# Kernel tuning notes

Measured on AMD Instinct MI355X. Metric: run time of the kernel, lower is better.

## Reference

```python
import jax, jax.numpy as jnp
import numpy as np

LEVEL_SHAPES = ((100, 100), (50, 50), (25, 25))  # (H, W) per feature level
B, S, D, H, L, P, FFN = 2, 13125, 256, 8, 3, 4, 1024
Dh = D // H


def setup_inputs() -> dict:
    key = jax.random.key(0)
    ks = jax.random.split(key, 24)

    def rn(k, shape, s=0.02):
        return jax.random.normal(k, shape, jnp.float32) * s

    starts = np.cumsum([0] + [h * w for h, w in LEVEL_SHAPES])[:-1]
    return {
        "x": jax.random.normal(ks[0], (B, S, D), jnp.float32),
        "pos_embed": jax.random.normal(ks[1], (B, S, D), jnp.float32) * 0.1,
        "ref_points": jax.random.uniform(ks[2], (B, S, L, 2), jnp.float32),
        "W_off": rn(ks[3], (D, H * L * P * 2)),
        "b_off": rn(ks[4], (H * L * P * 2,), 0.5),
        "W_attn": rn(ks[5], (D, H * L * P)),
        "b_attn": rn(ks[6], (H * L * P,)),
        "W_val": rn(ks[7], (D, D)),
        "b_val": rn(ks[8], (D,)),
        "W_out": rn(ks[9], (D, D)),
        "b_out": rn(ks[10], (D,)),
        "g1": jnp.ones((D,), jnp.float32),
        "be1": jnp.zeros((D,), jnp.float32),
        "W1": rn(ks[11], (D, FFN)),
        "b1": rn(ks[12], (FFN,)),
        "W2": rn(ks[13], (FFN, D)),
        "b2": rn(ks[14], (D,)),
        "g2": jnp.ones((D,), jnp.float32),
        "be2": jnp.zeros((D,), jnp.float32),
        "level_shapes": jnp.array(LEVEL_SHAPES, jnp.int32),
        "level_start_idx": jnp.array(starts, jnp.int32),
    }


def layer_norm(x, g, b, eps=1e-5):
    m = jnp.mean(x, -1, keepdims=True)
    v = jnp.var(x, -1, keepdims=True)
    return (x - m) * jax.lax.rsqrt(v + eps) * g + b


def bilinear_sample(vl, loc, Hl, Wl):
    # vl: [B,H,S_l,Dh]; loc: [B,H,S,P,2] normalized (x,y) in [0,1]
    # grid_sample semantics: align_corners=False, padding_mode='zeros'
    x = loc[..., 0] * Wl - 0.5
    y = loc[..., 1] * Hl - 0.5
    x0 = jnp.floor(x)
    y0 = jnp.floor(y)
    fx = x - x0
    fy = y - y0
    x0i = x0.astype(jnp.int32)
    y0i = y0.astype(jnp.int32)
    out = 0.0
    for dy, dx, w in ((0, 0, (1 - fx) * (1 - fy)), (0, 1, fx * (1 - fy)),
                      (1, 0, (1 - fx) * fy), (1, 1, fx * fy)):
        xi = x0i + dx
        yi = y0i + dy
        valid = (xi >= 0) & (xi < Wl) & (yi >= 0) & (yi < Hl)
        idx = jnp.clip(yi, 0, Hl - 1) * Wl + jnp.clip(xi, 0, Wl - 1)
        b_, h_, s_, p_ = idx.shape
        g = jnp.take_along_axis(vl, idx.reshape(b_, h_, s_ * p_)[..., None], axis=2)
        g = g.reshape(b_, h_, s_, p_, Dh)
        out = out + g * (w * valid)[..., None]
    return out  # [B,H,S,P,Dh]


def ms_deform_attn(q, x, ref_points, W_off, b_off, W_attn, b_attn, W_val, b_val, W_out, b_out):
    value = (x @ W_val + b_val).reshape(B, S, H, Dh).transpose(0, 2, 1, 3)  # [B,H,S,Dh]
    off = (q @ W_off + b_off).reshape(B, S, H, L, P, 2)
    attn = jax.nn.softmax((q @ W_attn + b_attn).reshape(B, S, H, L * P), axis=-1)
    attn = attn.reshape(B, S, H, L, P).transpose(0, 2, 1, 3, 4)  # [B,H,S,L,P]
    # offset normalizer is (W, H) per level
    norm = jnp.array([[w, h] for h, w in LEVEL_SHAPES], jnp.float32)
    loc = ref_points[:, :, None, :, None, :] + off / norm[None, None, None, :, None, :]
    loc = loc.transpose(0, 2, 1, 3, 4, 5)  # [B,H,S,L,P,2]
    s0 = 0
    sampled = []
    for l, (Hl, Wl) in enumerate(LEVEL_SHAPES):
        vl = jax.lax.slice_in_dim(value, s0, s0 + Hl * Wl, axis=2)
        sampled.append(bilinear_sample(vl, loc[:, :, :, l], Hl, Wl))
        s0 += Hl * Wl
    sampled = jnp.stack(sampled, axis=3)  # [B,H,S,L,P,Dh]
    out = jnp.einsum('bhslp,bhslpd->bshd', attn, sampled).reshape(B, S, D)
    return out @ W_out + b_out


def reference(x, pos_embed, ref_points, W_off, b_off, W_attn, b_attn, W_val, b_val,
              W_out, b_out, g1, be1, W1, b1, W2, b2, g2, be2,
              level_shapes, level_start_idx):
    q = x + pos_embed
    attn_out = ms_deform_attn(q, x, ref_points, W_off, b_off, W_attn, b_attn,
                              W_val, b_val, W_out, b_out)
    h1 = layer_norm(x + attn_out, g1, be1)
    ffn = jax.nn.relu(h1 @ W1 + b1) @ W2 + b2
    return layer_norm(h1 + ffn, g2, be2)
```

## Files before the change

### kernel.cpp

```cpp
#include <hip/hip_runtime.h>
#include <hip/hip_bf16.h>

namespace {

constexpr int kB = 2, kS = 13125, kD = 256, kH = 8, kL = 3, kP = 4, kFFN = 1024, kDh = 32;
constexpr int kM = kB * kS;

typedef __attribute__((ext_vector_type(8))) short short8v;
typedef __attribute__((ext_vector_type(4))) float f32x4;

__device__ __forceinline__ float bf2f(unsigned short u) {
  unsigned int x = ((unsigned int)u) << 16;
  return __builtin_bit_cast(float, x);
}
__device__ __forceinline__ unsigned short f2bf(float f) {
  unsigned int u = __builtin_bit_cast(unsigned int, f);
  u += 0x7FFFu + ((u >> 16) & 1u);
  return (unsigned short)(u >> 16);
}

__device__ __forceinline__ void gload_lds16(const void* g, void* l) {
  __builtin_amdgcn_global_load_lds(
      (const __attribute__((address_space(1))) unsigned int*)g,
      (__attribute__((address_space(3))) unsigned int*)l, 16, 0, 0);
}

__global__ __launch_bounds__(256) void wprep_kernel(const float* __restrict__ W,
                                                    unsigned short* __restrict__ Wt,
                                                    int K, int N, int total) {
  int idx = blockIdx.x * 256 + threadIdx.x;
  if (idx >= total) return;
  int n = idx / K, k = idx - n * K;
  float v = (n < N) ? W[(size_t)k * N + n] : 0.f;
  Wt[idx] = f2bf(v);
}

__global__ __launch_bounds__(256) void wprep_comb(const float* __restrict__ Woff,
                                                  const float* __restrict__ Wattn,
                                                  const float* __restrict__ boff,
                                                  const float* __restrict__ battn,
                                                  unsigned short* __restrict__ Wt,
                                                  float* __restrict__ bc) {
  int idx = blockIdx.x * 256 + threadIdx.x;
  if (idx >= 288 * 256) return;
  int n = idx >> 8, k = idx & 255;
  int h = n / 36, j = n - h * 36;
  float v = (j < 24) ? Woff[(size_t)k * 192 + h * 24 + j]
                     : Wattn[(size_t)k * 96 + h * 12 + (j - 24)];
  Wt[idx] = f2bf(v);
  if (idx < 288) {
    int hh = idx / 36, jj = idx - hh * 36;
    bc[idx] = (jj < 24) ? boff[hh * 24 + jj] : battn[hh * 12 + (jj - 24)];
  }
}

__global__ __launch_bounds__(256) void prep_kernel(const float4* __restrict__ x,
                                                   const float4* __restrict__ pos,
                                                   ushort4* __restrict__ xb,
                                                   ushort4* __restrict__ qb, int n4) {
  int i = blockIdx.x * 256 + threadIdx.x;
  if (i < n4) {
    float4 a = x[i], b = pos[i];
    xb[i] = make_ushort4(f2bf(a.x), f2bf(a.y), f2bf(a.z), f2bf(a.w));
    qb[i] = make_ushort4(f2bf(a.x + b.x), f2bf(a.y + b.y),
                         f2bf(a.z + b.z), f2bf(a.w + b.w));
  }
}

template <int EPI, bool OBF, int MI>
__global__ __launch_bounds__(256) void mfma_gemm(const unsigned short* __restrict__ A,
                                                 const unsigned short* __restrict__ Bt,
                                                 const float* __restrict__ bias,
                                                 void* __restrict__ Cp,
                                                 int M, int N, int K) {
  constexpr int BM = MI * 32;
  __shared__ unsigned short smem[2 * 128 * 32];
  unsigned short* As = smem;
  unsigned short* Bs = smem + BM * 32;
  const int tid = threadIdx.x;
  const int w = tid >> 6, lane = tid & 63;
  const int m0 = blockIdx.y * BM, n0 = blockIdx.x * 128;
  const int wr = w >> 1, wc = w & 1;
  const int r_ = lane >> 2, sl = lane & 3;

  f32x4 acc[MI][4] = {};

  for (int k0 = 0; k0 < K; k0 += 32) {
#pragma unroll
    for (int i = 0; i < MI / 2; ++i) {
      const int row = i * 64 + w * 16 + r_;
      const int sg = sl ^ ((row >> 1) & 3);
      int arow = m0 + row;
      arow = arow < M ? arow : M - 1;
      gload_lds16(A + (size_t)arow * K + k0 + sg * 8, &As[(i * 64 + w * 16) * 32]);
    }
#pragma unroll
    for (int i = 0; i < 2; ++i) {
      const int row = i * 64 + w * 16 + r_;
      const int sg = sl ^ ((row >> 1) & 3);
      gload_lds16(Bt + (size_t)(n0 + row) * K + k0 + sg * 8, &Bs[(i * 64 + w * 16) * 32]);
    }
    __syncthreads();
    short8v a[MI], b[4];
#pragma unroll
    for (int mi = 0; mi < MI; ++mi) {
      const int row = wr * (MI * 16) + mi * 16 + (lane & 15);
      const int slot = (lane >> 4) ^ ((row >> 1) & 3);
      a[mi] = *(const short8v*)&As[row * 32 + slot * 8];
    }
#pragma unroll
    for (int ni = 0; ni < 4; ++ni) {
      const int row = wc * 64 + ni * 16 + (lane & 15);
      const int slot = (lane >> 4) ^ ((row >> 1) & 3);
      b[ni] = *(const short8v*)&Bs[row * 32 + slot * 8];
    }
#pragma unroll
    for (int mi = 0; mi < MI; ++mi)
#pragma unroll
      for (int ni = 0; ni < 4; ++ni)
        acc[mi][ni] = __builtin_amdgcn_mfma_f32_16x16x32_bf16(a[mi], b[ni], acc[mi][ni], 0, 0, 0);
    __syncthreads();
  }

  const int cr = lane >> 4, cc = lane & 15;
  if (OBF) {
    unsigned short* Cs = smem;
#pragma unroll
    for (int half = 0; half < MI / 2; ++half) {
      if (MI == 2 || wr == half) {
#pragma unroll
        for (int ni = 0; ni < 4; ++ni) {
          const int col = wc * 64 + ni * 16 + cc;
          const float bv = bias[n0 + col];
#pragma unroll
          for (int mi = 0; mi < MI; ++mi)
#pragma unroll
            for (int r = 0; r < 4; ++r) {
              const int loc = wr * (MI * 16) + mi * 16 + cr * 4 + r - half * 64;
              float v = acc[mi][ni][r] + bv;
              if (EPI == 2) v = fmaxf(v, 0.f);
              const int ch = (col >> 3) ^ (loc & 7);
              Cs[loc * 128 + ch * 8 + (col & 7)] = f2bf(v);
            }
        }
      }
      __syncthreads();
      const int lr = tid >> 4, lc = tid & 15;
#pragma unroll
      for (int pp = 0; pp < 4; ++pp) {
        const int loc = pp * 16 + lr;
        const int grow = m0 + half * 64 + loc;
        const short8v vv = *(const short8v*)&Cs[loc * 128 + ((lc ^ (loc & 7)) * 8)];
        if (grow < M)
          *(short8v*)((unsigned short*)Cp + (size_t)grow * N + n0 + lc * 8) = vv;
      }
      __syncthreads();
    }
  } else {
#pragma unroll
    for (int ni = 0; ni < 4; ++ni) {
      const int col = n0 + wc * 64 + ni * 16 + cc;
      if (col >= N) continue;
      const float bv = bias[col];
#pragma unroll
      for (int mi = 0; mi < MI; ++mi) {
#pragma unroll
        for (int r = 0; r < 4; ++r) {
          const int row = m0 + wr * (MI * 16) + mi * 16 + cr * 4 + r;
          if (row >= M) continue;
          ((float*)Cp)[(size_t)row * N + col] = acc[mi][ni][r] + bv;
        }
      }
    }
  }
}

__global__ __launch_bounds__(256) void sample_kernel(const unsigned short* __restrict__ value,
                                                     const float* __restrict__ oa,
                                                     const float* __restrict__ refp,
                                                     unsigned short* __restrict__ out) {
  const int tid = threadIdx.x;
  const int sub = tid >> 2;
  const int lane = tid & 3;
  const int gi = blockIdx.x * 64 + sub;
  if (gi >= kB * kS * kH) return;
  const int h = gi & 7;
  const int bs = gi >> 3;
  const int b = (bs >= kS) ? 1 : 0;

  const float* op = oa + (size_t)bs * 288 + h * 36;
  const float* al = op + 24;
  float w[12];
  float mx = -1e30f;
#pragma unroll
  for (int i = 0; i < 12; ++i) { w[i] = al[i]; mx = fmaxf(mx, w[i]); }
  float sum = 0.f;
#pragma unroll
  for (int i = 0; i < 12; ++i) { w[i] = expf(w[i] - mx); sum += w[i]; }
  const float inv = 1.f / sum;
#pragma unroll
  for (int i = 0; i < 12; ++i) w[i] *= inv;

  const float* rp = refp + (size_t)bs * (kL * 2);
  const unsigned short* vbase = value + (size_t)b * kS * kD + h * kDh + lane * 8;

  const int LH[3] = {100, 50, 25}, LW[3] = {100, 50, 25}, LS[3] = {0, 10000, 12500};
  float acc[8] = {};
#pragma unroll
  for (int l = 0; l < 3; ++l) {
    const int Wi = LW[l], Hi = LH[l];
    const float Wl = (float)Wi, Hl = (float)Hi;
    const float rxw = rp[l * 2 + 0] * Wl - 0.5f;
    const float ryh = rp[l * 2 + 1] * Hl - 0.5f;
    const unsigned short* lvl = vbase + (size_t)LS[l] * kD;
#pragma unroll
    for (int p = 0; p < 4; ++p) {
      const float ox = op[l * 8 + p * 2 + 0], oy = op[l * 8 + p * 2 + 1];
      const float xf = rxw + ox;
      const float yf = ryh + oy;
      const float x0f = floorf(xf), y0f = floorf(yf);
      const float fx = xf - x0f, fy = yf - y0f;
      const int x0 = (int)x0f, y0 = (int)y0f;
      const int x1 = x0 + 1, y1 = y0 + 1;
      const bool vx0 = (unsigned)x0 < (unsigned)Wi;
      const bool vx1 = (unsigned)x1 < (unsigned)Wi;
      const bool vy0 = (unsigned)y0 < (unsigned)Hi;
      const bool vy1 = (unsigned)y1 < (unsigned)Hi;
      const int cx0 = min(max(x0, 0), Wi - 1), cx1 = min(max(x1, 0), Wi - 1);
      const int cy0 = min(max(y0, 0), Hi - 1), cy1 = min(max(y1, 0), Hi - 1);
      const float aw = w[l * 4 + p];
      const float ax = aw * fx, a0 = aw - ax;
      const float w00 = a0 - a0 * fy, w10 = a0 * fy;
      const float w01 = ax - ax * fy, w11 = ax * fy;
      const float m00 = (vx0 && vy0) ? w00 : 0.f;
      const float m01 = (vx1 && vy0) ? w01 : 0.f;
      const float m10 = (vx0 && vy1) ? w10 : 0.f;
      const float m11 = (vx1 && vy1) ? w11 : 0.f;
      const int ry0 = cy0 * Wi, ry1 = cy1 * Wi;
      const short8v q00 = *(const short8v*)(lvl + ((size_t)(ry0 + cx0) << 8));
      const short8v q01 = *(const short8v*)(lvl + ((size_t)(ry0 + cx1) << 8));
      const short8v q10 = *(const short8v*)(lvl + ((size_t)(ry1 + cx0) << 8));
      const short8v q11 = *(const short8v*)(lvl + ((size_t)(ry1 + cx1) << 8));
#pragma unroll
      for (int c = 0; c < 8; ++c) {
        float s = m00 * bf2f((unsigned short)q00[c]);
        s = fmaf(m01, bf2f((unsigned short)q01[c]), s);
        s = fmaf(m10, bf2f((unsigned short)q10[c]), s);
        s = fmaf(m11, bf2f((unsigned short)q11[c]), s);
        acc[c] += s;
      }
    }
  }
  unsigned short r[8];
#pragma unroll
  for (int c = 0; c < 8; ++c) r[c] = f2bf(acc[c]);
  *(short8v*)(out + (size_t)bs * kD + h * kDh + lane * 8) = *(const short8v*)r;
}

template <int WB>
__global__ __launch_bounds__(256) void lnres_kernel(const float* __restrict__ X,
                                                    const unsigned short* __restrict__ Ab,
                                                    const float* __restrict__ g,
                                                    const float* __restrict__ be,
                                                    float* __restrict__ out,
                                                    unsigned short* __restrict__ outb,
                                                    int rows) {
  const int wid = threadIdx.x >> 6, lane = threadIdx.x & 63;
  const int row = blockIdx.x * 4 + wid;
  if (row >= rows) return;
  const float4 v = ((const float4*)(X + (size_t)row * kD))[lane];
  const ushort4 a4 = ((const ushort4*)(Ab + (size_t)row * kD))[lane];
  float4 t;
  t.x = v.x + bf2f(a4.x);
  t.y = v.y + bf2f(a4.y);
  t.z = v.z + bf2f(a4.z);
  t.w = v.w + bf2f(a4.w);
  float s = t.x + t.y + t.z + t.w;
  float sq = t.x * t.x + t.y * t.y + t.z * t.z + t.w * t.w;
#pragma unroll
  for (int o = 1; o < 64; o <<= 1) {
    s += __shfl_xor(s, o);
    sq += __shfl_xor(sq, o);
  }
  const float mean = s * (1.f / kD);
  const float var = sq * (1.f / kD) - mean * mean;
  const float rs = rsqrtf(var + 1e-5f);
  const float4 gg = ((const float4*)g)[lane];
  const float4 bb = ((const float4*)be)[lane];
  float4 o4;
  o4.x = (t.x - mean) * rs * gg.x + bb.x;
  o4.y = (t.y - mean) * rs * gg.y + bb.y;
  o4.z = (t.z - mean) * rs * gg.z + bb.z;
  o4.w = (t.w - mean) * rs * gg.w + bb.w;
  ((float4*)(out + (size_t)row * kD))[lane] = o4;
  if (WB) {
    ((ushort4*)(outb + (size_t)row * kD))[lane] =
        make_ushort4(f2bf(o4.x), f2bf(o4.y), f2bf(o4.z), f2bf(o4.w));
  }
}

}

extern "C" void kernel_launch(void* const* d_in, const int* in_sizes, int n_in,
                              void* d_out, int out_size, void* d_ws, size_t ws_size,
                              hipStream_t stream) {
  const float* x      = (const float*)d_in[0];
  const float* pos    = (const float*)d_in[1];
  const float* refp   = (const float*)d_in[2];
  const float* W_off  = (const float*)d_in[3];
  const float* b_off  = (const float*)d_in[4];
  const float* W_attn = (const float*)d_in[5];
  const float* b_attn = (const float*)d_in[6];
  const float* W_val  = (const float*)d_in[7];
  const float* b_val  = (const float*)d_in[8];
  const float* W_out  = (const float*)d_in[9];
  const float* b_out  = (const float*)d_in[10];
  const float* g1     = (const float*)d_in[11];
  const float* be1    = (const float*)d_in[12];
  const float* W1     = (const float*)d_in[13];
  const float* b1     = (const float*)d_in[14];
  const float* W2     = (const float*)d_in[15];
  const float* b2     = (const float*)d_in[16];
  const float* g2     = (const float*)d_in[17];
  const float* be2    = (const float*)d_in[18];
  float* outp = (float*)d_out;

  char* ws = (char*)d_ws;
  unsigned short* Wvt = (unsigned short*)(ws + 0);
  unsigned short* Wot = (unsigned short*)(ws + 131072);
  unsigned short* Wct = (unsigned short*)(ws + 262144);
  float* bcomb        = (float*)(ws + 262144 + 288 * 512);
  unsigned short* W1t = (unsigned short*)(ws + 458752);
  unsigned short* W2t = (unsigned short*)(ws + 983040);
  const size_t MDb = (size_t)kM * kD * 2;
  char* regA = ws + 1507328;
  char* regB = regA + MDb;
  char* regC = regB + MDb;
  char* regG = regC + 43680000;
  char* regH = regG + (size_t)kM * kD * 4;

  unsigned short* xb    = (unsigned short*)regA;
  unsigned short* aob   = (unsigned short*)regA;
  unsigned short* qb    = (unsigned short*)regB;
  unsigned short* f2b   = (unsigned short*)regB;
  unsigned short* value = (unsigned short*)regC;
  float* oa   = (float*)(regC + MDb);
  float* h1   = (float*)regC;
  unsigned short* h1b = (unsigned short*)(regC + (size_t)kM * kD * 4);
  unsigned short* sv  = (unsigned short*)regG;
  unsigned short* h2b = (unsigned short*)regH;

  const dim3 blk(256);
  const int mt64 = (kM + 63) / 64;
  const int n4 = kM * kD / 4;

  wprep_kernel<<<(256 * 256 + 255) / 256, blk, 0, stream>>>(W_val, Wvt, 256, 256, 256 * 256);
  wprep_kernel<<<(256 * 256 + 255) / 256, blk, 0, stream>>>(W_out, Wot, 256, 256, 256 * 256);
  wprep_comb<<<288, blk, 0, stream>>>(W_off, W_attn, b_off, b_attn, Wct, bcomb);
  wprep_kernel<<<(1024 * 256 + 255) / 256, blk, 0, stream>>>(W1, W1t, 256, 1024, 1024 * 256);
  wprep_kernel<<<(256 * 1024 + 255) / 256, blk, 0, stream>>>(W2, W2t, 1024, 256, 256 * 1024);

  prep_kernel<<<(n4 + 255) / 256, blk, 0, stream>>>((const float4*)x, (const float4*)pos,
                                                    (ushort4*)xb, (ushort4*)qb, n4);
  mfma_gemm<0, true, 2><<<dim3(2, mt64), blk, 0, stream>>>(xb, Wvt, b_val, value,
                                                           kM, 256, 256);
  mfma_gemm<0, false, 2><<<dim3(3, mt64), blk, 0, stream>>>(qb, Wct, bcomb, oa,
                                                            kM, 288, 256);
  sample_kernel<<<(kB * kS * kH + 63) / 64, blk, 0, stream>>>(value, oa, refp, sv);
  mfma_gemm<0, true, 2><<<dim3(2, mt64), blk, 0, stream>>>(sv, Wot, b_out, aob,
                                                           kM, 256, 256);
  lnres_kernel<1><<<(kM + 3) / 4, blk, 0, stream>>>(x, aob, g1, be1, h1, h1b, kM);
  mfma_gemm<2, true, 2><<<dim3(8, mt64), blk, 0, stream>>>(h1b, W1t, b1, h2b,
                                                           kM, 1024, 256);
  mfma_gemm<0, true, 2><<<dim3(2, mt64), blk, 0, stream>>>(h2b, W2t, b2, f2b,
                                                           kM, 256, 1024);
  lnres_kernel<0><<<(kM + 3) / 4, blk, 0, stream>>>(h1, f2b, g2, be2, outp, nullptr, kM);
}
```

Measured before the change: 208.9 us.

## Fuse FFN GEMMs, store value in head-major layout, vectorize sampling

Replaces the two FFN GEMMs with a single fused kernel. Each block keeps a 64-row tile of h1 in LDS and loops over 64-wide hidden chunks, applying ReLU in LDS before feeding the second GEMM, so the 1024-wide intermediate never goes to global memory. The value projection now writes in [B,H,S,Dh] layout so the sampling gathers read contiguous per-head rows. The sampler also uses packed float2 accumulation and fast exp. The fused kernel reads W2 straight from global with no LDS staging and uses large LDS (about 80KB), which may lower occupancy.

Result: no change. 208.5 us (-0.2%).

```diff
diff --git a/kernel.cpp b/kernel.cpp
--- a/kernel.cpp
+++ b/kernel.cpp
@@ -8,6 +8,7 @@
 
 typedef __attribute__((ext_vector_type(8))) short short8v;
 typedef __attribute__((ext_vector_type(4))) float f32x4;
+typedef __attribute__((ext_vector_type(2))) float f32x2;
 
 __device__ __forceinline__ float bf2f(unsigned short u) {
   unsigned int x = ((unsigned int)u) << 16;
@@ -67,7 +68,7 @@
   }
 }
 
-template <int EPI, bool OBF, int MI>
+template <int EPI, bool OBF, int MI, bool VHM>
 __global__ __launch_bounds__(256) void mfma_gemm(const unsigned short* __restrict__ A,
                                                  const unsigned short* __restrict__ Bt,
                                                  const float* __restrict__ bias,
@@ -151,8 +152,18 @@
         const int loc = pp * 16 + lr;
         const int grow = m0 + half * 64 + loc;
         const short8v vv = *(const short8v*)&Cs[loc * 128 + ((lc ^ (loc & 7)) * 8)];
-        if (grow < M)
-          *(short8v*)((unsigned short*)Cp + (size_t)grow * N + n0 + lc * 8) = vv;
+        if (grow < M) {
+          if (VHM) {
+            const int col = n0 + lc * 8;
+            const int bb = grow >= kS ? 1 : 0;
+            const int ss = grow - bb * kS;
+            const int hh = col >> 5;
+            *(short8v*)((unsigned short*)Cp +
+                        (((size_t)(bb * kH + hh) * kS + ss) * kDh + (col & 31))) = vv;
+          } else {
+            *(short8v*)((unsigned short*)Cp + (size_t)grow * N + n0 + lc * 8) = vv;
+          }
+        }
       }
       __syncthreads();
     }
@@ -173,6 +184,121 @@
       }
     }
   }
+}
+
+__global__ __launch_bounds__(256) void ffn_fused(const unsigned short* __restrict__ Ain,
+                                                 const unsigned short* __restrict__ W1t,
+                                                 const unsigned short* __restrict__ W2t,
+                                                 const float* __restrict__ b1,
+                                                 const float* __restrict__ b2,
+                                                 unsigned short* __restrict__ Cp,
+                                                 int M) {
+  __shared__ unsigned short As[64 * 256];
+  __shared__ unsigned short W1s[64 * 256];
+  __shared__ unsigned short Ps[2][64 * 64];
+  const int tid = threadIdx.x;
+  const int w = tid >> 6, lane = tid & 63;
+  const int m0 = blockIdx.x * 64;
+  const int cr = lane >> 4, cc = lane & 15;
+
+#pragma unroll
+  for (int it = 0; it < 8; ++it) {
+    const int row = it * 8 + (tid >> 5);
+    const int ch = tid & 31;
+    int grow = m0 + row;
+    grow = grow < M ? grow : M - 1;
+    gload_lds16(Ain + (size_t)grow * 256 + (ch ^ (row & 7)) * 8, &As[row * 256 + ch * 8]);
+  }
+
+  f32x4 acc[4][4] = {};
+
+  for (int jt = 0; jt < 16; ++jt) {
+#pragma unroll
+    for (int it = 0; it < 8; ++it) {
+      const int row = it * 8 + (tid >> 5);
+      const int ch = tid & 31;
+      gload_lds16(W1t + (size_t)(jt * 64 + row) * 256 + (ch ^ (row & 7)) * 8,
+                  &W1s[row * 256 + ch * 8]);
+    }
+    __syncthreads();
+
+    f32x4 p1[4] = {};
+#pragma unroll
+    for (int kk = 0; kk < 8; ++kk) {
+      const int arow = w * 16 + cc;
+      const short8v av = *(const short8v*)&As[arow * 256 + (((kk * 4 + cr) ^ (arow & 7)) * 8)];
+#pragma unroll
+      for (int ni = 0; ni < 4; ++ni) {
+        const int brow = ni * 16 + cc;
+        const short8v bv = *(const short8v*)&W1s[brow * 256 + (((kk * 4 + cr) ^ (brow & 7)) * 8)];
+        p1[ni] = __builtin_amdgcn_mfma_f32_16x16x32_bf16(av, bv, p1[ni], 0, 0, 0);
+      }
+    }
+    unsigned short* P = Ps[jt & 1];
+#pragma unroll
+    for (int ni = 0; ni < 4; ++ni) {
+      const int col = ni * 16 + cc;
+      const float bv = b1[jt * 64 + col];
+#pragma unroll
+      for (int r = 0; r < 4; ++r) {
+        const int prow = w * 16 + cr * 4 + r;
+        const float v = fmaxf(p1[ni][r] + bv, 0.f);
+        P[prow * 64 + (((col >> 3) ^ (prow & 7)) * 8) + (col & 7)] = f2bf(v);
+      }
+    }
+    __syncthreads();
+
+#pragma unroll
+    for (int kk = 0; kk < 2; ++kk) {
+#pragma unroll
+      for (int mi = 0; mi < 4; ++mi) {
+        const int prow = mi * 16 + cc;
+        const short8v av = *(const short8v*)&P[prow * 64 + (((kk * 4 + cr) ^ (prow & 7)) * 8)];
+#pragma unroll
+        for (int ni = 0; ni < 4; ++ni) {
+          const int ncol = w * 64 + ni * 16 + cc;
+          const short8v bv = *(const short8v*)(W2t + (size_t)ncol * 1024 + jt * 64 + kk * 32 + cr * 8);
+          acc[mi][ni] = __builtin_amdgcn_mfma_f32_16x16x32_bf16(av, bv, acc[mi][ni], 0, 0, 0);
+        }
+      }
+    }
+  }
+
+#pragma unroll
+  for (int ni = 0; ni < 4; ++ni) {
+    const int col = w * 64 + ni * 16 + cc;
+    const float bv = b2[col];
+#pragma unroll
+    for (int mi = 0; mi < 4; ++mi)
+#pragma unroll
+      for (int r = 0; r < 4; ++r) {
+        const int row = mi * 16 + cr * 4 + r;
+        const float v = acc[mi][ni][r] + bv;
+        As[row * 256 + (((col >> 3) ^ (row & 7)) * 8) + (col & 7)] = f2bf(v);
+      }
+  }
+  __syncthreads();
+#pragma unroll
+  for (int it = 0; it < 8; ++it) {
+    const int row = it * 8 + (tid >> 5);
+    const int grow = m0 + row;
+    const int ch = tid & 31;
+    const short8v vv = *(const short8v*)&As[row * 256 + ((ch ^ (row & 7)) * 8)];
+    if (grow < M) *(short8v*)(Cp + (size_t)grow * 256 + ch * 8) = vv;
+  }
+}
+
+__device__ __forceinline__ void acc2u(f32x2* acc, unsigned u, int i, float m) {
+  f32x2 v;
+  v.x = __builtin_bit_cast(float, u << 16);
+  v.y = __builtin_bit_cast(float, u & 0xFFFF0000u);
+  acc[i] += m * v;
+}
+__device__ __forceinline__ void acc_corner(f32x2* acc, uint4 q, float m) {
+  acc2u(acc, q.x, 0, m);
+  acc2u(acc, q.y, 1, m);
+  acc2u(acc, q.z, 2, m);
+  acc2u(acc, q.w, 3, m);
 }
 
 __global__ __launch_bounds__(256) void sample_kernel(const unsigned short* __restrict__ value,
@@ -196,23 +322,23 @@
   for (int i = 0; i < 12; ++i) { w[i] = al[i]; mx = fmaxf(mx, w[i]); }
   float sum = 0.f;
 #pragma unroll
-  for (int i = 0; i < 12; ++i) { w[i] = expf(w[i] - mx); sum += w[i]; }
+  for (int i = 0; i < 12; ++i) { w[i] = __expf(w[i] - mx); sum += w[i]; }
   const float inv = 1.f / sum;
 #pragma unroll
   for (int i = 0; i < 12; ++i) w[i] *= inv;
 
   const float* rp = refp + (size_t)bs * (kL * 2);
-  const unsigned short* vbase = value + (size_t)b * kS * kD + h * kDh + lane * 8;
+  const unsigned short* vbase = value + ((size_t)(b * kH + h) * kS) * kDh + lane * 8;
 
   const int LH[3] = {100, 50, 25}, LW[3] = {100, 50, 25}, LS[3] = {0, 10000, 12500};
-  float acc[8] = {};
+  f32x2 acc[4] = {};
 #pragma unroll
   for (int l = 0; l < 3; ++l) {
     const int Wi = LW[l], Hi = LH[l];
     const float Wl = (float)Wi, Hl = (float)Hi;
     const float rxw = rp[l * 2 + 0] * Wl - 0.5f;
     const float ryh = rp[l * 2 + 1] * Hl - 0.5f;
-    const unsigned short* lvl = vbase + (size_t)LS[l] * kD;
+    const unsigned short* lvl = vbase + (size_t)LS[l] * kDh;
 #pragma unroll
     for (int p = 0; p < 4; ++p) {
       const float ox = op[l * 8 + p * 2 + 0], oy = op[l * 8 + p * 2 + 1];
@@ -237,23 +363,22 @@
       const float m10 = (vx0 && vy1) ? w10 : 0.f;
       const float m11 = (vx1 && vy1) ? w11 : 0.f;
       const int ry0 = cy0 * Wi, ry1 = cy1 * Wi;
-      const short8v q00 = *(const short8v*)(lvl + ((size_t)(ry0 + cx0) << 8));
-      const short8v q01 = *(const short8v*)(lvl + ((size_t)(ry0 + cx1) << 8));
-      const short8v q10 = *(const short8v*)(lvl + ((size_t)(ry1 + cx0) << 8));
-      const short8v q11 = *(const short8v*)(lvl + ((size_t)(ry1 + cx1) << 8));
-#pragma unroll
-      for (int c = 0; c < 8; ++c) {
-        float s = m00 * bf2f((unsigned short)q00[c]);
-        s = fmaf(m01, bf2f((unsigned short)q01[c]), s);
-        s = fmaf(m10, bf2f((unsigned short)q10[c]), s);
-        s = fmaf(m11, bf2f((unsigned short)q11[c]), s);
-        acc[c] += s;
-      }
+      const uint4 q00 = *(const uint4*)(lvl + (size_t)(ry0 + cx0) * kDh);
+      const uint4 q01 = *(const uint4*)(lvl + (size_t)(ry0 + cx1) * kDh);
+      const uint4 q10 = *(const uint4*)(lvl + (size_t)(ry1 + cx0) * kDh);
+      const uint4 q11 = *(const uint4*)(lvl + (size_t)(ry1 + cx1) * kDh);
+      acc_corner(acc, q00, m00);
+      acc_corner(acc, q01, m01);
+      acc_corner(acc, q10, m10);
+      acc_corner(acc, q11, m11);
     }
   }
   unsigned short r[8];
 #pragma unroll
-  for (int c = 0; c < 8; ++c) r[c] = f2bf(acc[c]);
+  for (int i = 0; i < 4; ++i) {
+    r[2 * i] = f2bf(acc[i].x);
+    r[2 * i + 1] = f2bf(acc[i].y);
+  }
   *(short8v*)(out + (size_t)bs * kD + h * kDh + lane * 8) = *(const short8v*)r;
 }
 
@@ -337,7 +462,6 @@
   char* regB = regA + MDb;
   char* regC = regB + MDb;
   char* regG = regC + 43680000;
-  char* regH = regG + (size_t)kM * kD * 4;
 
   unsigned short* xb    = (unsigned short*)regA;
   unsigned short* aob   = (unsigned short*)regA;
@@ -348,7 +472,6 @@
   float* h1   = (float*)regC;
   unsigned short* h1b = (unsigned short*)(regC + (size_t)kM * kD * 4);
   unsigned short* sv  = (unsigned short*)regG;
-  unsigned short* h2b = (unsigned short*)regH;
 
   const dim3 blk(256);
   const int mt64 = (kM + 63) / 64;
@@ -362,17 +485,14 @@
 
   prep_kernel<<<(n4 + 255) / 256, blk, 0, stream>>>((const float4*)x, (const float4*)pos,
                                                     (ushort4*)xb, (ushort4*)qb, n4);
-  mfma_gemm<0, true, 2><<<dim3(2, mt64), blk, 0, stream>>>(xb, Wvt, b_val, value,
-                                                           kM, 256, 256);
-  mfma_gemm<0, false, 2><<<dim3(3, mt64), blk, 0, stream>>>(qb, Wct, bcomb, oa,
-                                                            kM, 288, 256);
+  mfma_gemm<0, true, 2, true><<<dim3(2, mt64), blk, 0, stream>>>(xb, Wvt, b_val, value,
+                                                                 kM, 256, 256);
+  mfma_gemm<0, false, 2, false><<<dim3(3, mt64), blk, 0, stream>>>(qb, Wct, bcomb, oa,
+                                                                   kM, 288, 256);
   sample_kernel<<<(kB * kS * kH + 63) / 64, blk, 0, stream>>>(value, oa, refp, sv);
-  mfma_gemm<0, true, 2><<<dim3(2, mt64), blk, 0, stream>>>(sv, Wot, b_out, aob,
-                                                           kM, 256, 256);
+  mfma_gemm<0, true, 2, false><<<dim3(2, mt64), blk, 0, stream>>>(sv, Wot, b_out, aob,
+                                                                  kM, 256, 256);
   lnres_kernel<1><<<(kM + 3) / 4, blk, 0, stream>>>(x, aob, g1, be1, h1, h1b, kM);
-  mfma_gemm<2, true, 2><<<dim3(8, mt64), blk, 0, stream>>>(h1b, W1t, b1, h2b,
-                                                           kM, 1024, 256);
-  mfma_gemm<0, true, 2><<<dim3(2, mt64), blk, 0, stream>>>(h2b, W2t, b2, f2b,
-                                                           kM, 256, 1024);
+  ffn_fused<<<mt64, blk, 0, stream>>>(h1b, W1t, W2t, b1, b2, f2b, kM);
   lnres_kernel<0><<<(kM + 3) / 4, blk, 0, stream>>>(h1, f2b, g2, be2, outp, nullptr, kM);
 }
```
